# Kernel tuning notes

Measured on AMD Instinct MI355X. Metric: run time of the kernel, lower is better.

The kernel has to match this reference:

```python
import jax, jax.numpy as jnp
import numpy as np

EPS = 1e-5

def hard_sigmoid(x):
    return jnp.clip(0.2 * x + 0.5, 0.0, 1.0)

def ln(x, g, b):
    m = jnp.mean(x, axis=-1, keepdims=True)
    std = jnp.sqrt(jnp.var(x, axis=-1, keepdims=True) + EPS)
    return g * ((x - m) / (std + EPS)) + b

def setup_inputs() -> dict:
    key = jax.random.key(0)
    k0, k1, k2 = jax.random.split(key, 3)
    B, T, I, H = 128, 128, 512, 512
    D = I + H
    x = jax.random.normal(k0, (B, T, I), dtype=jnp.float32)
    mask = jnp.ones((B, T), dtype=jnp.int32)
    W = jax.random.normal(k1, (D, H + 1), dtype=jnp.float32) * 0.02
    U = jax.random.normal(k2, (D, H + 1), dtype=jnp.float32) * 0.02
    b = jnp.zeros((H + 1,), dtype=jnp.float32)
    gammas = jnp.ones((2, H + 1), dtype=jnp.float32)
    betas = jnp.zeros((2, H + 1), dtype=jnp.float32)
    return {"x": x, "mask": mask, "W": W, "U": U, "b": b,
            "gammas": gammas, "betas": betas,
            "bucket_size": 128, "depth": 4, "input_dim": 512}

def reference(x, mask, W, U, b, gammas, betas, bucket_size, depth, input_dim):
    B, T, I = x.shape
    H = W.shape[1] - 1
    D = I + H
    # pad input to (input_dim | hidden_dim) layout, time-major, truncate to bucket
    xp = jnp.concatenate([x, jnp.zeros((B, T, H), x.dtype)], axis=-1)
    xs = jnp.transpose(xp, (1, 0, 2))[:bucket_size]          # (Tb, B, D)
    m = (mask.T[:bucket_size] > 0)                            # (Tb, B) bool
    first = jnp.zeros((1, B), dtype=bool)
    shift = jnp.concatenate([m[1:], first], axis=0)
    m2 = m & (~shift)
    m2 = jnp.concatenate([first, m2[:-1]], axis=0)            # (Tb, B)
    Tb = xs.shape[0]
    g0, g1 = gammas[0], gammas[1]
    b0, b1 = betas[0], betas[1]

    def hstep(carry, inp):
        h_tm1, fk_tm1, hv_tm1 = carry
        x_t, fkp_tm1, fkp, mk, mk2, hvp = inp
        sum2 = ln(h_tm1 @ U, g1, b1)                          # (B, H+1)
        s = ln(x_t @ W, g0, b0) + sum2 + b                    # (B, H+1)
        fk_both = hard_sigmoid(s[:, 0])
        fk_t1 = hard_sigmoid(sum2[:, 0] + b[0])
        fk = fkp_tm1 + (1 - fkp_tm1) * (fk_tm1 * fk_both + (1 - fk_tm1) * fk_t1)
        fk = jnp.where(mk2, 0.0, fk)
        h_core = jnp.tanh(s[:, 1:])                           # (B, H)
        h_new = jnp.concatenate([jnp.zeros((B, I), x_t.dtype), h_core], axis=-1)
        h_only = hv_tm1 * fk * (fkp + (1 - fkp) * (1 - hvp))
        x_only = hvp * (1 - fkp) * (1 - fk + fk * (1 - hv_tm1))
        both = (1 - fkp) * fk * hv_tm1 * hvp
        h = h_only[:, None] * h_tm1 + x_only[:, None] * x_t + both[:, None] * h_new
        hv = 1 - (1 - h_only) * (1 - x_only) * (1 - both)
        h = jnp.where(mk[:, None], h, h_tm1)
        fk = jnp.where(mk, fk, fk_tm1)
        hv = jnp.where(mk, hv, hv_tm1)
        fk = jnp.where(mk2, 0.0, fk)
        return (h, fk, hv), (h, fk, hv)

    def vstep(carry, _):
        xv, fkp_tm1, fkp, hvp = carry
        init = (jnp.zeros((B, D), x.dtype),
                jnp.zeros((B,), x.dtype),
                jnp.zeros((B,), x.dtype))
        _, (h_seq, fk_seq, hv_seq) = jax.lax.scan(hstep, init, (xv, fkp_tm1, fkp, m, m2, hvp))
        shifted = jnp.concatenate([fk_seq[1:], jnp.zeros((1, B), x.dtype)], axis=0)
        return (h_seq, fk_seq, shifted, hv_seq), None

    carry0 = (xs,
              jnp.zeros((Tb, B), x.dtype),
              jnp.zeros((Tb, B), x.dtype),
              jnp.ones((Tb, B), x.dtype))
    (h_final, _, _, _), _ = jax.lax.scan(vstep, carry0, None, length=depth)
    return h_final[-1][:, I:]                                  # (B, H)
```

## Files before the change

### kernel.cpp

```cpp
#include <hip/hip_runtime.h>
#include <cstdint>

#define TT 128
#define BB 128
#define II 512
#define HH 512
#define DD 1024
#define NC 513
#define NPAD 520
#define NT 36
#define EPSL 1e-5f

typedef short    s8v  __attribute__((ext_vector_type(8)));
typedef float    f4v  __attribute__((ext_vector_type(4)));
typedef _Float16 h2v  __attribute__((ext_vector_type(2)));

__device__ __forceinline__ ushort f2bf(float f){
  uint u = __builtin_bit_cast(uint, f);
  uint r = (u + 0x7fffu + ((u >> 16) & 1u)) >> 16;
  return (ushort)r;
}
__device__ __forceinline__ float bf2f(ushort s){
  uint u = ((uint)s) << 16;
  return __builtin_bit_cast(float, u);
}
__device__ __forceinline__ float hsig(float x){
  return fminf(fmaxf(0.2f * x + 0.5f, 0.f), 1.f);
}
__device__ __forceinline__ float ftanh(float x){
  float ax = fminf(fabsf(x), 15.f);
  float e  = __builtin_amdgcn_exp2f(ax * 2.885390082f);
  float r  = (e - 1.f) * __builtin_amdgcn_rcpf(e + 1.f);
  return __builtin_copysignf(r, x);
}
__device__ __forceinline__ float dot2(uint a, uint b, float c){
#if __has_builtin(__builtin_amdgcn_fdot2)
  return __builtin_amdgcn_fdot2(__builtin_bit_cast(h2v, a),
                                __builtin_bit_cast(h2v, b), c, false);
#else
  h2v x = __builtin_bit_cast(h2v, a), y = __builtin_bit_cast(h2v, b);
  return fmaf((float)x[1], (float)y[1], fmaf((float)x[0], (float)y[0], c));
#endif
}

__global__ void prepack_B(const float* __restrict__ src, ushort* __restrict__ dst){
  int idx = blockIdx.x * 256 + threadIdx.x;
  if (idx >= 128 * NT * 16 * 8) return;
  int kl = idx & 7;
  int ni = (idx >> 3) & 15;
  int nt = (idx >> 7) % NT;
  int kc = idx / (NT * 16 * 8);
  int k = kc * 8 + kl;
  int n = nt * 16 + ni;
  float v = (n < NC) ? src[k * NC + n] : 0.f;
  dst[idx] = f2bf(v);
}

__global__ void prepack_Uhi_pk(const float* __restrict__ U, uint* __restrict__ dst,
                               float* __restrict__ ucol){
  int idx = blockIdx.x * 256 + threadIdx.x;
  if (idx < 64 * 512 * 4){
    int j = idx & 3;
    int n = (idx >> 2) & 511;
    int c = idx >> 11;
    int k0 = II + 8 * c + 2 * j;
    _Float16 lo = (_Float16)U[(size_t)k0 * NC + n];
    _Float16 hi = (_Float16)U[(size_t)(k0 + 1) * NC + n];
    dst[idx] = (uint)__builtin_bit_cast(ushort, lo)
             | ((uint)__builtin_bit_cast(ushort, hi) << 16);
  }
  if (idx < 512) ucol[idx] = U[(size_t)(II + idx) * NC + 512];
}

__global__ __launch_bounds__(1024) void gemm_ln(
    const float* __restrict__ A, int amode, int ksteps,
    const ushort* __restrict__ Bpk, ushort* __restrict__ out,
    int do_ln, const float* __restrict__ gam, const float* __restrict__ bet,
    const float* __restrict__ bias)
{
  __shared__ ushort As[64][40];
  __shared__ float red[4][4][16][2];
  int tid = threadIdx.x;
  int lane = tid & 63, wid = tid >> 6;
  int quad = lane >> 4, l16 = lane & 15;
  int wm = wid >> 2, wn = wid & 3;
  int blk = blockIdx.x;

  f4v acc[9];
#pragma unroll
  for (int i = 0; i < 9; i++) acc[i] = (f4v){0.f, 0.f, 0.f, 0.f};

  int arow = tid >> 4;
  int acp  = tid & 15;
  int r = blk * 64 + arow;
  const float* aptr;
  if (amode == 0){ int t = r >> 7, b = r & 127; aptr = A + ((size_t)(b * TT + t)) * II + acp * 2; }
  else           { aptr = A + (size_t)r * DD + acp * 2; }

  for (int ks = 0; ks < ksteps; ks++){
    __syncthreads();
    float2 a2 = *(const float2*)(aptr + ks * 32);
    uint pk = (uint)f2bf(a2.x) | ((uint)f2bf(a2.y) << 16);
    *(uint*)&As[arow][acp * 2] = pk;
    __syncthreads();
    s8v af = *(const s8v*)&As[wm * 16 + l16][quad * 8];
    int kc = ks * 4 + quad;
    const s8v* bp = (const s8v*)Bpk + (size_t)kc * (NT * 16) + l16;
#pragma unroll
    for (int i = 0; i < 9; i++){
      s8v bf = bp[(wn * 9 + i) * 16];
      acc[i] = __builtin_amdgcn_mfma_f32_16x16x32_bf16(af, bf, acc[i], 0, 0, 0);
    }
  }

  int rowbase = blk * 64 + wm * 16 + quad * 4;
  if (do_ln){
    float s1[4], s2[4];
#pragma unroll
    for (int g = 0; g < 4; g++){
      float a = 0.f, q = 0.f;
#pragma unroll
      for (int i = 0; i < 9; i++){ float v = acc[i][g]; a += v; q += v * v; }
#pragma unroll
      for (int m = 1; m < 16; m <<= 1){ a += __shfl_xor(a, m, 64); q += __shfl_xor(q, m, 64); }
      s1[g] = a; s2[g] = q;
    }
    if (l16 == 0){
#pragma unroll
      for (int g = 0; g < 4; g++){
        red[wm][wn][quad * 4 + g][0] = s1[g];
        red[wm][wn][quad * 4 + g][1] = s2[g];
      }
    }
    __syncthreads();
#pragma unroll
    for (int g = 0; g < 4; g++){
      int rr = quad * 4 + g;
      float S1 = red[wm][0][rr][0] + red[wm][1][rr][0] + red[wm][2][rr][0] + red[wm][3][rr][0];
      float S2 = red[wm][0][rr][1] + red[wm][1][rr][1] + red[wm][2][rr][1] + red[wm][3][rr][1];
      float mean = S1 * (1.f / 513.f);
      float var  = S2 * (1.f / 513.f) - mean * mean;
      float inv  = 1.f / (sqrtf(var + EPSL) + EPSL);
      size_t rg = (size_t)(rowbase + g);
#pragma unroll
      for (int i = 0; i < 9; i++){
        int n = wn * 144 + i * 16 + l16;
        if (n < NC){
          float val = gam[n] * ((acc[i][g] - mean) * inv) + bet[n] + bias[n];
          out[rg * NPAD + n] = f2bf(val);
        }
      }
    }
  } else {
#pragma unroll
    for (int g = 0; g < 4; g++){
      size_t rg = (size_t)(rowbase + g);
#pragma unroll
      for (int i = 0; i < 9; i++){
        int n = wn * 144 + i * 16 + l16;
        if (n < NC) out[rg * NPAD + n] = f2bf(acc[i][g]);
      }
    }
  }
}

__global__ __launch_bounds__(512) void rnn_layer(
    int layer,
    const float* __restrict__ x,
    float* __restrict__ h_seq,
    const ushort* __restrict__ lnXW,
    ushort* __restrict__ vbuf,
    float* __restrict__ fkbuf,
    float* __restrict__ hvbuf,
    const uint* __restrict__ Upk4,
    const float* __restrict__ ucol,
    const int* __restrict__ mask,
    const float* __restrict__ gam1, const float* __restrict__ bet1,
    const float* __restrict__ bias,
    float* __restrict__ out)
{
  __shared__ __align__(16) ushort tanh16[512];
  __shared__ __align__(16) float  tanhvf[512];
  __shared__ float red_a[8], red_q[8], red_p[8];
  __shared__ float sh_v0;
  __shared__ int msk[TT];

  int tid = threadIdx.x;
  int b = blockIdx.x;
  int lane = tid & 63, wid = tid >> 6;
  const bool lastL = (layer == 3);

  float sv = 0.f;
  float v512 = 0.f;
  float h_lo = 0.f, h_hi = 0.f;
  float fkc = 0.f, hvc = 0.f;
  float g1n = gam1[tid], b1n = bet1[tid];
  float g10 = gam1[0],  b10 = bet1[0];
  float g1e = gam1[512], b1e = bet1[512];
  float bias0 = bias[0];
  float uc = ucol[tid];
  float ho_p = 0.f, xo_p = 0.f, bo_p = 0.f, xu5_p = 0.f;
  int mk_p = 0;

  if (tid < TT) msk[tid] = mask[b * TT + tid];
  if (lane == 0){ red_a[wid] = 0.f; red_q[wid] = 0.f; red_p[wid] = 0.f; }
  if (tid == 0) sh_v0 = 0.f;
  __syncthreads();

  for (int t = 0; t < TT; t++){
    size_t row = (size_t)(t * BB + b);

    float lw    = bf2f(lnXW[row * NPAD + tid]);
    float lw0   = bf2f(lnXW[row * NPAD]);
    float lw512 = bf2f(lnXW[row * NPAD + 512]);
    float xu    = bf2f(vbuf[row * NPAD + tid]);
    float xu5   = bf2f(vbuf[row * NPAD + 512]);
    float xlo, xhi;
    if (layer == 0){ xlo = x[((size_t)(b * TT + t)) * II + tid]; xhi = 0.f; }
    else { xlo = h_seq[row * DD + tid]; xhi = h_seq[row * DD + 512 + tid]; }
    float fkp_tm1 = 0.f, fkp = 0.f, hvp = 1.f;
    if (layer > 0){
      fkp_tm1 = fkbuf[t * BB + b];
      fkp = (t + 1 < TT) ? fkbuf[(t + 1) * BB + b] : 0.f;
      hvp = hvbuf[t * BB + b];
    }
    int mraw  = msk[t];
    int mprev = (t > 0) ? msk[t - 1] : 0;

    if (t > 0){
      float y512 = red_p[0] + red_p[1] + red_p[2] + red_p[3]
                 + red_p[4] + red_p[5] + red_p[6] + red_p[7];
      float nv5 = ho_p * v512 + xo_p * xu5_p + bo_p * y512;
      if (mk_p) v512 = nv5;
      if (tid == 0 && !lastL) vbuf[(row - BB) * NPAD + 512] = f2bf(v512);
    }
    float S = red_a[0] + red_a[1] + red_a[2] + red_a[3]
            + red_a[4] + red_a[5] + red_a[6] + red_a[7];
    float Q = red_q[0] + red_q[1] + red_q[2] + red_q[3]
            + red_q[4] + red_q[5] + red_q[6] + red_q[7];
    S += v512; Q += v512 * v512;
    float v0 = sh_v0;
    float mean = S * (1.f / 513.f);
    float var  = Q * (1.f / 513.f) - mean * mean;
    float inv  = 1.f / (sqrtf(var + EPSL) + EPSL);

    bool mk  = mraw > 0;
    bool mk2 = (t > 0) && (mprev > 0) && !mk;
    float sum20 = (v0 - mean) * inv * g10 + b10;
    float s0 = lw0 + sum20;
    float fk_both = hsig(s0);
    float fk_t1   = hsig(sum20 + bias0);
    float fk = fkp_tm1 + (1.f - fkp_tm1) * (fkc * fk_both + (1.f - fkc) * fk_t1);
    if (mk2) fk = 0.f;
    float h_only = hvc * fk * (fkp + (1.f - fkp) * (1.f - hvp));
    float x_only = hvp * (1.f - fkp) * (1.f - fk + fk * (1.f - hvc));
    float both   = (1.f - fkp) * fk * hvc * hvp;
    float hv = 1.f - (1.f - h_only) * (1.f - x_only) * (1.f - both);
    fkc = mk ? fk : fkc;
    hvc = mk ? hv : hvc;
    if (mk2) fkc = 0.f;

    {
      float sum2 = (sv - mean) * inv * g1n + b1n;
      float s = lw + sum2;
      float th = ftanh(s);
      if (tid == 0){
        float sum2e = (v512 - mean) * inv * g1e + b1e;
        float the = ftanh(lw512 + sum2e);
        tanh16[511] = __builtin_bit_cast(ushort, (_Float16)the);
        tanhvf[511] = the;
      } else {
        tanh16[tid - 1] = __builtin_bit_cast(ushort, (_Float16)th);
        tanhvf[tid - 1] = th;
      }
    }
    __syncthreads();

    float y0 = 0.f, y1 = 0.f, y2 = 0.f, y3 = 0.f;
    {
      const uint4* up = (const uint4*)Upk4 + tid;
      const uint4* tp = (const uint4*)tanh16;
#pragma unroll 16
      for (int c = 0; c < 64; c++){
        uint4 uu = up[(size_t)c * 512];
        uint4 tt = tp[c];
        y0 = dot2(tt.x, uu.x, y0);
        y1 = dot2(tt.y, uu.y, y1);
        y2 = dot2(tt.z, uu.z, y2);
        y3 = dot2(tt.w, uu.w, y3);
      }
    }
    float y = (y0 + y1) + (y2 + y3);
    {
      float p = tanhvf[tid] * uc;
#pragma unroll
      for (int m = 1; m < 64; m <<= 1) p += __shfl_xor(p, m, 64);
      if (lane == 0) red_p[wid] = p;
    }

    float nv = h_only * sv + x_only * xu + both * y;
    if (mk) sv = nv;
    float thh = tanhvf[tid];
    float nh_lo = h_only * h_lo + x_only * xlo;
    float nh_hi = h_only * h_hi + x_only * xhi + both * thh;
    if (mk){ h_lo = nh_lo; h_hi = nh_hi; }
    if (!lastL){
      vbuf[row * NPAD + tid] = f2bf(sv);
      h_seq[row * DD + tid] = h_lo;
      h_seq[row * DD + 512 + tid] = h_hi;
      if (tid == 0){ fkbuf[t * BB + b] = fkc; hvbuf[t * BB + b] = hvc; }
    }
    if (lastL && t == TT - 1) out[b * HH + tid] = h_hi;

    ho_p = h_only; xo_p = x_only; bo_p = both; mk_p = mk ? 1 : 0; xu5_p = xu5;

    {
      float a = sv, q = sv * sv;
#pragma unroll
      for (int m = 1; m < 64; m <<= 1){ a += __shfl_xor(a, m, 64); q += __shfl_xor(q, m, 64); }
      if (lane == 0){ red_a[wid] = a; red_q[wid] = q; }
      if (tid == 0) sh_v0 = sv;
    }
    __syncthreads();
  }

  if (tid == 0 && !lastL){
    float y512 = red_p[0] + red_p[1] + red_p[2] + red_p[3]
               + red_p[4] + red_p[5] + red_p[6] + red_p[7];
    float nv5 = ho_p * v512 + xo_p * xu5_p + bo_p * y512;
    if (mk_p) v512 = nv5;
    vbuf[(size_t)((TT - 1) * BB + b) * NPAD + 512] = f2bf(v512);
  }
}

extern "C" void kernel_launch(void* const* d_in, const int* in_sizes, int n_in,
                              void* d_out, int out_size, void* d_ws, size_t ws_size,
                              hipStream_t stream)
{
  (void)in_sizes; (void)n_in; (void)out_size; (void)ws_size;
  const float* x      = (const float*)d_in[0];
  const int*   mask   = (const int*)d_in[1];
  const float* W      = (const float*)d_in[2];
  const float* U      = (const float*)d_in[3];
  const float* bias   = (const float*)d_in[4];
  const float* gammas = (const float*)d_in[5];
  const float* betas  = (const float*)d_in[6];
  float* out = (float*)d_out;

  char* ws = (char*)d_ws;
  size_t off = 0;
  auto alloc = [&](size_t bytes) -> void* {
    void* p = ws + off;
    off += (bytes + 255) & ~(size_t)255;
    return p;
  };
  float*  h_seq = (float*) alloc((size_t)TT * BB * DD * 4);
  ushort* lnXW  = (ushort*)alloc((size_t)TT * BB * NPAD * 2);
  ushort* vbuf  = (ushort*)alloc((size_t)TT * BB * NPAD * 2);
  float*  fkbuf = (float*) alloc((size_t)TT * BB * 4);
  float*  hvbuf = (float*) alloc((size_t)TT * BB * 4);
  ushort* Wpk   = (ushort*)alloc((size_t)128 * NT * 16 * 8 * 2);
  ushort* Upk   = (ushort*)alloc((size_t)128 * NT * 16 * 8 * 2);
  uint*   Upk4  = (uint*)  alloc((size_t)64 * 512 * 4 * 4);
  float*  ucol  = (float*) alloc(512 * 4);

  int npk = 128 * NT * 16 * 8;
  prepack_B<<<dim3((npk + 255) / 256), dim3(256), 0, stream>>>(W, Wpk);
  prepack_B<<<dim3((npk + 255) / 256), dim3(256), 0, stream>>>(U, Upk);
  prepack_Uhi_pk<<<dim3((64 * 512 * 4 + 255) / 256), dim3(256), 0, stream>>>(U, Upk4, ucol);

  const float* g0 = gammas,      *g1 = gammas + NC;
  const float* be0 = betas,      *be1 = betas + NC;

  gemm_ln<<<dim3(256), dim3(1024), 0, stream>>>(x, 0, 16, Wpk, lnXW, 1, g0, be0, bias);
  gemm_ln<<<dim3(256), dim3(1024), 0, stream>>>(x, 0, 16, Upk, vbuf, 0, g0, be0, bias);
  rnn_layer<<<dim3(BB), dim3(512), 0, stream>>>(0, x, h_seq, lnXW, vbuf, fkbuf, hvbuf,
                                                Upk4, ucol, mask, g1, be1, bias, out);
  for (int d = 1; d < 4; d++){
    gemm_ln<<<dim3(256), dim3(1024), 0, stream>>>(h_seq, 1, 32, Wpk, lnXW, 1, g0, be0, bias);
    rnn_layer<<<dim3(BB), dim3(512), 0, stream>>>(d, x, h_seq, lnXW, vbuf, fkbuf, hvbuf,
                                                  Upk4, ucol, mask, g1, be1, bias, out);
  }
}
```

Measured before the change: 3.036 ms.

## Process two batch rows per RNN block to share U weight loads

Each rnn_layer block now handles two batch elements, so every packed U chunk loaded from global memory feeds two dot products instead of one, halving U traffic per sequence. The grid shrinks from 128 to 64 blocks, and reductions for both rows are merged into one shuffle pass with a shared reduction array. The cost is fewer blocks on a GPU with many CUs, more registers per thread, and twice the serial elementwise work per step.

Measured after the change: 5.710 ms. 88.1% more time.

```diff
diff --git a/kernel.cpp b/kernel.cpp
--- a/kernel.cpp
+++ b/kernel.cpp
@@ -179,157 +179,231 @@
     const float* __restrict__ bias,
     float* __restrict__ out)
 {
-  __shared__ __align__(16) ushort tanh16[512];
-  __shared__ __align__(16) float  tanhvf[512];
-  __shared__ float red_a[8], red_q[8], red_p[8];
-  __shared__ float sh_v0;
-  __shared__ int msk[TT];
+  __shared__ __align__(16) ushort tanhA[512], tanhB[512];
+  __shared__ __align__(16) float  tvfA[512],  tvfB[512];
+  __shared__ float redS[8][6];
+  __shared__ float sh_v0A, sh_v0B;
+  __shared__ int mskA[TT], mskB[TT];
 
   int tid = threadIdx.x;
-  int b = blockIdx.x;
+  int bA = 2 * blockIdx.x, bB = bA + 1;
   int lane = tid & 63, wid = tid >> 6;
   const bool lastL = (layer == 3);
 
-  float sv = 0.f;
-  float v512 = 0.f;
-  float h_lo = 0.f, h_hi = 0.f;
-  float fkc = 0.f, hvc = 0.f;
+  float svA = 0.f, svB = 0.f;
+  float v5A = 0.f, v5B = 0.f;
+  float hloA = 0.f, hloB = 0.f, hhiA = 0.f, hhiB = 0.f;
+  float fkcA = 0.f, fkcB = 0.f, hvcA = 0.f, hvcB = 0.f;
+  float hoA = 0.f, xoA = 0.f, boA = 0.f, xu5pA = 0.f; int mkpA = 0;
+  float hoB = 0.f, xoB = 0.f, boB = 0.f, xu5pB = 0.f; int mkpB = 0;
+
   float g1n = gam1[tid], b1n = bet1[tid];
   float g10 = gam1[0],  b10 = bet1[0];
   float g1e = gam1[512], b1e = bet1[512];
   float bias0 = bias[0];
   float uc = ucol[tid];
-  float ho_p = 0.f, xo_p = 0.f, bo_p = 0.f, xu5_p = 0.f;
-  int mk_p = 0;
-
-  if (tid < TT) msk[tid] = mask[b * TT + tid];
-  if (lane == 0){ red_a[wid] = 0.f; red_q[wid] = 0.f; red_p[wid] = 0.f; }
-  if (tid == 0) sh_v0 = 0.f;
+
+  if (tid < TT) mskA[tid] = mask[bA * TT + tid];
+  else if (tid < 2 * TT) mskB[tid - TT] = mask[bB * TT + (tid - TT)];
+  if (lane == 0){
+#pragma unroll
+    for (int i = 0; i < 6; i++) redS[wid][i] = 0.f;
+  }
+  if (tid == 0){ sh_v0A = 0.f; sh_v0B = 0.f; }
   __syncthreads();
 
   for (int t = 0; t < TT; t++){
-    size_t row = (size_t)(t * BB + b);
-
-    float lw    = bf2f(lnXW[row * NPAD + tid]);
-    float lw0   = bf2f(lnXW[row * NPAD]);
-    float lw512 = bf2f(lnXW[row * NPAD + 512]);
-    float xu    = bf2f(vbuf[row * NPAD + tid]);
-    float xu5   = bf2f(vbuf[row * NPAD + 512]);
-    float xlo, xhi;
-    if (layer == 0){ xlo = x[((size_t)(b * TT + t)) * II + tid]; xhi = 0.f; }
-    else { xlo = h_seq[row * DD + tid]; xhi = h_seq[row * DD + 512 + tid]; }
-    float fkp_tm1 = 0.f, fkp = 0.f, hvp = 1.f;
+    size_t rowA = (size_t)(t * BB + bA);
+    size_t rowB = (size_t)(t * BB + bB);
+
+    float lwA = bf2f(lnXW[rowA * NPAD + tid]);
+    float lwB = bf2f(lnXW[rowB * NPAD + tid]);
+    float lw0A = bf2f(lnXW[rowA * NPAD]);
+    float lw0B = bf2f(lnXW[rowB * NPAD]);
+    float lw5A = bf2f(lnXW[rowA * NPAD + 512]);
+    float lw5B = bf2f(lnXW[rowB * NPAD + 512]);
+    float xuA = bf2f(vbuf[rowA * NPAD + tid]);
+    float xuB = bf2f(vbuf[rowB * NPAD + tid]);
+    float xu5A = bf2f(vbuf[rowA * NPAD + 512]);
+    float xu5B = bf2f(vbuf[rowB * NPAD + 512]);
+    float xloA, xhiA, xloB, xhiB;
+    if (layer == 0){
+      xloA = x[((size_t)(bA * TT + t)) * II + tid]; xhiA = 0.f;
+      xloB = x[((size_t)(bB * TT + t)) * II + tid]; xhiB = 0.f;
+    } else {
+      xloA = h_seq[rowA * DD + tid]; xhiA = h_seq[rowA * DD + 512 + tid];
+      xloB = h_seq[rowB * DD + tid]; xhiB = h_seq[rowB * DD + 512 + tid];
+    }
+    float fkpA = 0.f, fknA = 0.f, hvpA = 1.f;
+    float fkpB = 0.f, fknB = 0.f, hvpB = 1.f;
     if (layer > 0){
-      fkp_tm1 = fkbuf[t * BB + b];
-      fkp = (t + 1 < TT) ? fkbuf[(t + 1) * BB + b] : 0.f;
-      hvp = hvbuf[t * BB + b];
-    }
-    int mraw  = msk[t];
-    int mprev = (t > 0) ? msk[t - 1] : 0;
+      fkpA = fkbuf[t * BB + bA];
+      fknA = (t + 1 < TT) ? fkbuf[(t + 1) * BB + bA] : 0.f;
+      hvpA = hvbuf[t * BB + bA];
+      fkpB = fkbuf[t * BB + bB];
+      fknB = (t + 1 < TT) ? fkbuf[(t + 1) * BB + bB] : 0.f;
+      hvpB = hvbuf[t * BB + bB];
+    }
+    int mrawA = mskA[t], mprevA = (t > 0) ? mskA[t - 1] : 0;
+    int mrawB = mskB[t], mprevB = (t > 0) ? mskB[t - 1] : 0;
 
     if (t > 0){
-      float y512 = red_p[0] + red_p[1] + red_p[2] + red_p[3]
-                 + red_p[4] + red_p[5] + red_p[6] + red_p[7];
-      float nv5 = ho_p * v512 + xo_p * xu5_p + bo_p * y512;
-      if (mk_p) v512 = nv5;
-      if (tid == 0 && !lastL) vbuf[(row - BB) * NPAD + 512] = f2bf(v512);
-    }
-    float S = red_a[0] + red_a[1] + red_a[2] + red_a[3]
-            + red_a[4] + red_a[5] + red_a[6] + red_a[7];
-    float Q = red_q[0] + red_q[1] + red_q[2] + red_q[3]
-            + red_q[4] + red_q[5] + red_q[6] + red_q[7];
-    S += v512; Q += v512 * v512;
-    float v0 = sh_v0;
-    float mean = S * (1.f / 513.f);
-    float var  = Q * (1.f / 513.f) - mean * mean;
-    float inv  = 1.f / (sqrtf(var + EPSL) + EPSL);
-
-    bool mk  = mraw > 0;
-    bool mk2 = (t > 0) && (mprev > 0) && !mk;
-    float sum20 = (v0 - mean) * inv * g10 + b10;
-    float s0 = lw0 + sum20;
-    float fk_both = hsig(s0);
-    float fk_t1   = hsig(sum20 + bias0);
-    float fk = fkp_tm1 + (1.f - fkp_tm1) * (fkc * fk_both + (1.f - fkc) * fk_t1);
-    if (mk2) fk = 0.f;
-    float h_only = hvc * fk * (fkp + (1.f - fkp) * (1.f - hvp));
-    float x_only = hvp * (1.f - fkp) * (1.f - fk + fk * (1.f - hvc));
-    float both   = (1.f - fkp) * fk * hvc * hvp;
-    float hv = 1.f - (1.f - h_only) * (1.f - x_only) * (1.f - both);
-    fkc = mk ? fk : fkc;
-    hvc = mk ? hv : hvc;
-    if (mk2) fkc = 0.f;
+      float y5A = 0.f, y5B = 0.f;
+#pragma unroll
+      for (int w = 0; w < 8; w++){ y5A += redS[w][2]; y5B += redS[w][5]; }
+      float nA = hoA * v5A + xoA * xu5pA + boA * y5A;
+      float nB = hoB * v5B + xoB * xu5pB + boB * y5B;
+      if (mkpA) v5A = nA;
+      if (mkpB) v5B = nB;
+      if (tid == 0 && !lastL){
+        vbuf[(rowA - BB) * NPAD + 512] = f2bf(v5A);
+        vbuf[(rowB - BB) * NPAD + 512] = f2bf(v5B);
+      }
+    }
+    float SA = 0.f, QA = 0.f, SB = 0.f, QB = 0.f;
+#pragma unroll
+    for (int w = 0; w < 8; w++){
+      SA += redS[w][0]; QA += redS[w][1];
+      SB += redS[w][3]; QB += redS[w][4];
+    }
+    SA += v5A; QA += v5A * v5A;
+    SB += v5B; QB += v5B * v5B;
+    float v0A = sh_v0A, v0B = sh_v0B;
+    float meanA = SA * (1.f / 513.f);
+    float varA  = QA * (1.f / 513.f) - meanA * meanA;
+    float invA  = 1.f / (sqrtf(varA + EPSL) + EPSL);
+    float meanB = SB * (1.f / 513.f);
+    float varB  = QB * (1.f / 513.f) - meanB * meanB;
+    float invB  = 1.f / (sqrtf(varB + EPSL) + EPSL);
+
+    bool mkA  = mrawA > 0;
+    bool mk2A = (t > 0) && (mprevA > 0) && !mkA;
+    bool mkB  = mrawB > 0;
+    bool mk2B = (t > 0) && (mprevB > 0) && !mkB;
+
+    float s20A = (v0A - meanA) * invA * g10 + b10;
+    float fkbA = hsig(lw0A + s20A);
+    float ft1A = hsig(s20A + bias0);
+    float fkA = fkpA + (1.f - fkpA) * (fkcA * fkbA + (1.f - fkcA) * ft1A);
+    if (mk2A) fkA = 0.f;
+    float h_oA = hvcA * fkA * (fknA + (1.f - fknA) * (1.f - hvpA));
+    float x_oA = hvpA * (1.f - fknA) * (1.f - fkA + fkA * (1.f - hvcA));
+    float boA_ = (1.f - fknA) * fkA * hvcA * hvpA;
+    float hvA = 1.f - (1.f - h_oA) * (1.f - x_oA) * (1.f - boA_);
+    fkcA = mkA ? fkA : fkcA;
+    hvcA = mkA ? hvA : hvcA;
+    if (mk2A) fkcA = 0.f;
+
+    float s20B = (v0B - meanB) * invB * g10 + b10;
+    float fkbB = hsig(lw0B + s20B);
+    float ft1B = hsig(s20B + bias0);
+    float fkB = fkpB + (1.f - fkpB) * (fkcB * fkbB + (1.f - fkcB) * ft1B);
+    if (mk2B) fkB = 0.f;
+    float h_oB = hvcB * fkB * (fknB + (1.f - fknB) * (1.f - hvpB));
+    float x_oB = hvpB * (1.f - fknB) * (1.f - fkB + fkB * (1.f - hvcB));
+    float boB_ = (1.f - fknB) * fkB * hvcB * hvpB;
+    float hvB = 1.f - (1.f - h_oB) * (1.f - x_oB) * (1.f - boB_);
+    fkcB = mkB ? fkB : fkcB;
+    hvcB = mkB ? hvB : hvcB;
+    if (mk2B) fkcB = 0.f;
 
     {
-      float sum2 = (sv - mean) * inv * g1n + b1n;
-      float s = lw + sum2;
-      float th = ftanh(s);
+      float thA = ftanh(lwA + (svA - meanA) * invA * g1n + b1n);
+      float thB = ftanh(lwB + (svB - meanB) * invB * g1n + b1n);
       if (tid == 0){
-        float sum2e = (v512 - mean) * inv * g1e + b1e;
-        float the = ftanh(lw512 + sum2e);
-        tanh16[511] = __builtin_bit_cast(ushort, (_Float16)the);
-        tanhvf[511] = the;
+        float theA = ftanh(lw5A + (v5A - meanA) * invA * g1e + b1e);
+        float theB = ftanh(lw5B + (v5B - meanB) * invB * g1e + b1e);
+        tanhA[511] = __builtin_bit_cast(ushort, (_Float16)theA);
+        tanhB[511] = __builtin_bit_cast(ushort, (_Float16)theB);
+        tvfA[511] = theA; tvfB[511] = theB;
       } else {
-        tanh16[tid - 1] = __builtin_bit_cast(ushort, (_Float16)th);
-        tanhvf[tid - 1] = th;
+        tanhA[tid - 1] = __builtin_bit_cast(ushort, (_Float16)thA);
+        tanhB[tid - 1] = __builtin_bit_cast(ushort, (_Float16)thB);
+        tvfA[tid - 1] = thA; tvfB[tid - 1] = thB;
       }
     }
     __syncthreads();
 
-    float y0 = 0.f, y1 = 0.f, y2 = 0.f, y3 = 0.f;
+    float yA0 = 0.f, yA1 = 0.f, yA2 = 0.f, yA3 = 0.f;
+    float yB0 = 0.f, yB1 = 0.f, yB2 = 0.f, yB3 = 0.f;
     {
       const uint4* up = (const uint4*)Upk4 + tid;
-      const uint4* tp = (const uint4*)tanh16;
-#pragma unroll 16
+      const uint4* ta = (const uint4*)tanhA;
+      const uint4* tb = (const uint4*)tanhB;
+#pragma unroll 8
       for (int c = 0; c < 64; c++){
         uint4 uu = up[(size_t)c * 512];
-        uint4 tt = tp[c];
-        y0 = dot2(tt.x, uu.x, y0);
-        y1 = dot2(tt.y, uu.y, y1);
-        y2 = dot2(tt.z, uu.z, y2);
-        y3 = dot2(tt.w, uu.w, y3);
-      }
-    }
-    float y = (y0 + y1) + (y2 + y3);
+        uint4 t1 = ta[c];
+        uint4 t2 = tb[c];
+        yA0 = dot2(t1.x, uu.x, yA0);  yB0 = dot2(t2.x, uu.x, yB0);
+        yA1 = dot2(t1.y, uu.y, yA1);  yB1 = dot2(t2.y, uu.y, yB1);
+        yA2 = dot2(t1.z, uu.z, yA2);  yB2 = dot2(t2.z, uu.z, yB2);
+        yA3 = dot2(t1.w, uu.w, yA3);  yB3 = dot2(t2.w, uu.w, yB3);
+      }
+    }
+    float yA = (yA0 + yA1) + (yA2 + yA3);
+    float yB = (yB0 + yB1) + (yB2 + yB3);
+
+    float thhA = tvfA[tid], thhB = tvfB[tid];
+    float nvA = h_oA * svA + x_oA * xuA + boA_ * yA;
+    float nvB = h_oB * svB + x_oB * xuB + boB_ * yB;
+    if (mkA) svA = nvA;
+    if (mkB) svB = nvB;
+    float nhloA = h_oA * hloA + x_oA * xloA;
+    float nhhiA = h_oA * hhiA + x_oA * xhiA + boA_ * thhA;
+    if (mkA){ hloA = nhloA; hhiA = nhhiA; }
+    float nhloB = h_oB * hloB + x_oB * xloB;
+    float nhhiB = h_oB * hhiB + x_oB * xhiB + boB_ * thhB;
+    if (mkB){ hloB = nhloB; hhiB = nhhiB; }
+    if (!lastL){
+      vbuf[rowA * NPAD + tid] = f2bf(svA);
+      vbuf[rowB * NPAD + tid] = f2bf(svB);
+      h_seq[rowA * DD + tid] = hloA;
+      h_seq[rowA * DD + 512 + tid] = hhiA;
+      h_seq[rowB * DD + tid] = hloB;
+      h_seq[rowB * DD + 512 + tid] = hhiB;
+      if (tid == 0){
+        fkbuf[t * BB + bA] = fkcA; hvbuf[t * BB + bA] = hvcA;
+        fkbuf[t * BB + bB] = fkcB; hvbuf[t * BB + bB] = hvcB;
+      }
+    }
+    if (lastL && t == TT - 1){
+      out[bA * HH + tid] = hhiA;
+      out[bB * HH + tid] = hhiB;
+    }
+
+    hoA = h_oA; xoA = x_oA; boA = boA_; mkpA = mkA ? 1 : 0; xu5pA = xu5A;
+    hoB = h_oB; xoB = x_oB; boB = boB_; mkpB = mkB ? 1 : 0; xu5pB = xu5B;
+
     {
-      float p = tanhvf[tid] * uc;
-#pragma unroll
-      for (int m = 1; m < 64; m <<= 1) p += __shfl_xor(p, m, 64);
-      if (lane == 0) red_p[wid] = p;
-    }
-
-    float nv = h_only * sv + x_only * xu + both * y;
-    if (mk) sv = nv;
-    float thh = tanhvf[tid];
-    float nh_lo = h_only * h_lo + x_only * xlo;
-    float nh_hi = h_only * h_hi + x_only * xhi + both * thh;
-    if (mk){ h_lo = nh_lo; h_hi = nh_hi; }
-    if (!lastL){
-      vbuf[row * NPAD + tid] = f2bf(sv);
-      h_seq[row * DD + tid] = h_lo;
-      h_seq[row * DD + 512 + tid] = h_hi;
-      if (tid == 0){ fkbuf[t * BB + b] = fkc; hvbuf[t * BB + b] = hvc; }
-    }
-    if (lastL && t == TT - 1) out[b * HH + tid] = h_hi;
-
-    ho_p = h_only; xo_p = x_only; bo_p = both; mk_p = mk ? 1 : 0; xu5_p = xu5;
-
-    {
-      float a = sv, q = sv * sv;
-#pragma unroll
-      for (int m = 1; m < 64; m <<= 1){ a += __shfl_xor(a, m, 64); q += __shfl_xor(q, m, 64); }
-      if (lane == 0){ red_a[wid] = a; red_q[wid] = q; }
-      if (tid == 0) sh_v0 = sv;
+      float aA = svA, qA = svA * svA, pA = thhA * uc;
+      float aB = svB, qB = svB * svB, pB = thhB * uc;
+#pragma unroll
+      for (int m = 1; m < 64; m <<= 1){
+        aA += __shfl_xor(aA, m, 64); qA += __shfl_xor(qA, m, 64);
+        pA += __shfl_xor(pA, m, 64);
+        aB += __shfl_xor(aB, m, 64); qB += __shfl_xor(qB, m, 64);
+        pB += __shfl_xor(pB, m, 64);
+      }
+      if (lane == 0){
+        redS[wid][0] = aA; redS[wid][1] = qA; redS[wid][2] = pA;
+        redS[wid][3] = aB; redS[wid][4] = qB; redS[wid][5] = pB;
+      }
+      if (tid == 0){ sh_v0A = svA; sh_v0B = svB; }
     }
     __syncthreads();
   }
 
   if (tid == 0 && !lastL){
-    float y512 = red_p[0] + red_p[1] + red_p[2] + red_p[3]
-               + red_p[4] + red_p[5] + red_p[6] + red_p[7];
-    float nv5 = ho_p * v512 + xo_p * xu5_p + bo_p * y512;
-    if (mk_p) v512 = nv5;
-    vbuf[(size_t)((TT - 1) * BB + b) * NPAD + 512] = f2bf(v512);
+    float y5A = 0.f, y5B = 0.f;
+#pragma unroll
+    for (int w = 0; w < 8; w++){ y5A += redS[w][2]; y5B += redS[w][5]; }
+    float nA = hoA * v5A + xoA * xu5pA + boA * y5A;
+    float nB = hoB * v5B + xoB * xu5pB + boB * y5B;
+    if (mkpA) v5A = nA;
+    if (mkpB) v5B = nB;
+    vbuf[(size_t)((TT - 1) * BB + bA) * NPAD + 512] = f2bf(v5A);
+    vbuf[(size_t)((TT - 1) * BB + bB) * NPAD + 512] = f2bf(v5B);
   }
 }
 
@@ -374,11 +448,11 @@
 
   gemm_ln<<<dim3(256), dim3(1024), 0, stream>>>(x, 0, 16, Wpk, lnXW, 1, g0, be0, bias);
   gemm_ln<<<dim3(256), dim3(1024), 0, stream>>>(x, 0, 16, Upk, vbuf, 0, g0, be0, bias);
-  rnn_layer<<<dim3(BB), dim3(512), 0, stream>>>(0, x, h_seq, lnXW, vbuf, fkbuf, hvbuf,
-                                                Upk4, ucol, mask, g1, be1, bias, out);
+  rnn_layer<<<dim3(BB / 2), dim3(512), 0, stream>>>(0, x, h_seq, lnXW, vbuf, fkbuf, hvbuf,
+                                                    Upk4, ucol, mask, g1, be1, bias, out);
   for (int d = 1; d < 4; d++){
     gemm_ln<<<dim3(256), dim3(1024), 0, stream>>>(h_seq, 1, 32, Wpk, lnXW, 1, g0, be0, bias);
-    rnn_layer<<<dim3(BB), dim3(512), 0, stream>>>(d, x, h_seq, lnXW, vbuf, fkbuf, hvbuf,
-                                                  Upk4, ucol, mask, g1, be1, bias, out);
-  }
-}
+    rnn_layer<<<dim3(BB / 2), dim3(512), 0, stream>>>(d, x, h_seq, lnXW, vbuf, fkbuf, hvbuf,
+                                                      Upk4, ucol, mask, g1, be1, bias, out);
+  }
+}
```
